# Performance work log

Hardware: AMD Instinct MI355X
Metric: run time of the kernel (lower is better)

The kernel has to match this reference:

```python
import jax, jax.numpy as jnp
import numpy as np

N = 100000
E = 1600000
F_IN = 128
H = 128


def setup_inputs() -> dict:
    key = jax.random.key(0)
    ks = jax.random.split(key, 12)
    x = jax.random.normal(ks[0], (N, F_IN), dtype=jnp.float32)
    edge_index = jax.random.randint(ks[1], (2, E), 0, N, dtype=jnp.int64)
    s = 1.0 / np.sqrt(F_IN)
    sh = 1.0 / np.sqrt(H)
    inp = {"x": x, "edge_index": edge_index}
    # SAGEConv params: lin_l (neighbor agg, with bias), lin_r (root, no bias)
    inp["W1l"] = jax.random.uniform(ks[2], (H, F_IN), jnp.float32, -s, s)
    inp["b1"] = jnp.zeros((H,), jnp.float32)
    inp["W1r"] = jax.random.uniform(ks[3], (H, F_IN), jnp.float32, -s, s)
    inp["W2l"] = jax.random.uniform(ks[4], (H, H), jnp.float32, -sh, sh)
    inp["b2"] = jnp.zeros((H,), jnp.float32)
    inp["W2r"] = jax.random.uniform(ks[5], (H, H), jnp.float32, -sh, sh)
    inp["W3l"] = jax.random.uniform(ks[6], (H, H), jnp.float32, -sh, sh)
    inp["b3"] = jnp.zeros((H,), jnp.float32)
    inp["W3r"] = jax.random.uniform(ks[7], (H, H), jnp.float32, -sh, sh)
    inp["Wo"] = jax.random.uniform(ks[8], (1, H), jnp.float32, -sh, sh)
    inp["bo"] = jnp.zeros((1,), jnp.float32)
    return inp


def _sage_max(h, src, dst, Wl, bl, Wr):
    # max-aggregate source features at destination nodes (empty -> 0, as PyG)
    m = jax.ops.segment_max(h[src], dst, num_segments=N)  # [N, d]
    m = jnp.where(jnp.isfinite(m), m, jnp.zeros_like(m))
    return m @ Wl.T + bl + h @ Wr.T


def reference(x, edge_index, W1l, b1, W1r, W2l, b2, W2r, W3l, b3, W3r, Wo, bo):
    src, dst = edge_index[0], edge_index[1]
    h1 = jax.nn.elu(_sage_max(x, src, dst, W1l, b1, W1r))
    h2 = jax.nn.elu(_sage_max(h1, src, dst, W2l, b2, W2r)) + h1
    h3 = jax.nn.elu(_sage_max(h2, src, dst, W3l, b3, W3r)) + h2
    return jax.nn.sigmoid(h3 @ Wo.T + bo)  # [N, 1]
```

## Files before the change

kernel.cpp:

```cpp
#include <hip/hip_runtime.h>
#include <hip/hip_fp16.h>
#include <math.h>

#define HDIM 128

#define BSHIFT 7
#define BW 128
#define BCAP 4096
#define NBKMAX 1024
#define CHUNK 4096

typedef __attribute__((ext_vector_type(8))) _Float16 f16x8;
typedef __attribute__((ext_vector_type(2))) _Float16 f16x2;
typedef __attribute__((ext_vector_type(16))) float f32x16;
typedef unsigned int uint32;
typedef unsigned short u16;

__device__ __forceinline__ uint32 hmax2u(uint32 a, uint32 b) {
    f16x2 ha = __builtin_bit_cast(f16x2, a);
    f16x2 hb = __builtin_bit_cast(f16x2, b);
    f16x2 r = __builtin_elementwise_max(ha, hb);
    return __builtin_bit_cast(uint32, r);
}
__device__ __forceinline__ uint32 hadd2u(uint32 a, uint32 b) {
    f16x2 ha = __builtin_bit_cast(f16x2, a);
    f16x2 hb = __builtin_bit_cast(f16x2, b);
    f16x2 r = ha + hb;
    return __builtin_bit_cast(uint32, r);
}


__global__ __launch_bounds__(256) void bucket_bin(
    const int* __restrict__ ei, int E_, int nbk,
    int* __restrict__ bucketCnt, uint32* __restrict__ tmp)
{
    __shared__ int cnt[NBKMAX];
    __shared__ int gbase[NBKMAX];
    const int t = threadIdx.x;
    const int start = blockIdx.x * CHUNK;
    const int end = min(start + CHUNK, E_);

    for (int i = t; i < nbk; i += 256) cnt[i] = 0;
    __syncthreads();
    for (int e = start + t; e < end; e += 256)
        atomicAdd(&cnt[ei[E_ + e] >> BSHIFT], 1);
    __syncthreads();
    for (int i = t; i < nbk; i += 256) {
        int c = cnt[i];
        gbase[i] = c ? atomicAdd(&bucketCnt[i], c) : 0;
    }
    __syncthreads();
    for (int i = t; i < nbk; i += 256) cnt[i] = 0;
    __syncthreads();
    for (int e = start + t; e < end; e += 256) {
        int d = ei[E_ + e];
        int s = ei[e];
        int b = d >> BSHIFT;
        int r = atomicAdd(&cnt[b], 1);
        tmp[(size_t)b * BCAP + gbase[b] + r] =
            ((uint32)(d & (BW - 1)) << 17) | (uint32)s;
    }
}

__global__ __launch_bounds__(1024) void bucket_scan(
    const int* __restrict__ bucketCnt, int* __restrict__ bucketBase,
    int nbk, int* __restrict__ off, int N_, int E_) {
    __shared__ int sd[1024];
    int t = threadIdx.x;
    int v = (t < nbk) ? bucketCnt[t] : 0;
    sd[t] = v;
    __syncthreads();
    for (int ofs = 1; ofs < 1024; ofs <<= 1) {
        int add = (t >= ofs) ? sd[t - ofs] : 0;
        __syncthreads();
        sd[t] += add;
        __syncthreads();
    }
    if (t < nbk) bucketBase[t] = sd[t] - v;
    if (t == 0) off[N_] = E_;
}

__global__ __launch_bounds__(256) void bucket_csr(
    const uint32* __restrict__ tmp, const int* __restrict__ bucketCnt,
    const int* __restrict__ bucketBase,
    int* __restrict__ off, int* __restrict__ srcs, int N_)
{
    __shared__ int lc[BW];
    __shared__ int lo[BW];
    __shared__ int sd[256];
    const int b = blockIdx.x, t = threadIdx.x;
    const int cnt = bucketCnt[b], base = bucketBase[b];
    const uint32* tp = tmp + (size_t)b * BCAP;

    if (t < BW) lc[t] = 0;
    __syncthreads();
    for (int i = t; i < cnt; i += 256) atomicAdd(&lc[tp[i] >> 17], 1);
    __syncthreads();

    int v = (t < BW) ? lc[t] : 0;
    sd[t] = v;
    __syncthreads();
    for (int ofs = 1; ofs < 256; ofs <<= 1) {
        int add = (t >= ofs) ? sd[t - ofs] : 0;
        __syncthreads();
        sd[t] += add;
        __syncthreads();
    }
    if (t < BW) lo[t] = sd[t] - v;
    __syncthreads();

    for (int i = t; i < BW; i += 256) {
        int node = b * BW + i;
        if (node < N_) off[node] = base + lo[i];
    }
    if (t < BW) lc[t] = lo[t];
    __syncthreads();
    for (int i = t; i < cnt; i += 256) {
        uint32 p = tp[i];
        int dl = p >> 17, s = p & 0x1FFFF;
        int pos = base + atomicAdd(&lc[dl], 1);
        srcs[pos] = s;
    }
}


__global__ void cast_x(const float* __restrict__ x, uint32* __restrict__ xb, int n2) {
    int i = blockIdx.x * 256 + threadIdx.x;
    if (i >= n2) return;
    float2 v = ((const float2*)x)[i];
    f16x2 h = { (_Float16)v.x, (_Float16)v.y };
    xb[i] = __builtin_bit_cast(uint32, h);
}

__global__ void cast_weights_packed(
    const float* __restrict__ W1l, const float* __restrict__ W1r,
    const float* __restrict__ W2l, const float* __restrict__ W2r,
    const float* __restrict__ W3l, const float* __restrict__ W3r,
    f16x8* __restrict__ PW)
{
    int tid = blockIdx.x * 256 + threadIdx.x;
    if (tid >= 3 * 4096) return;
    int layer = tid >> 12, rem = tid & 4095;
    int g = rem >> 10, ks = (rem >> 6) & 15, lane = rem & 63;
    int col = g * 32 + (lane & 31), kq = lane >> 5;
    const float* src;
    if (layer == 0)      src = (ks < 8) ? W1l : W1r;
    else if (layer == 1) src = (ks < 8) ? W2l : W2r;
    else                 src = (ks < 8) ? W3l : W3r;
    int kk = (ks & 7) * 16 + kq * 8;
    f16x8 v;
#pragma unroll
    for (int j = 0; j < 8; ++j) v[j] = (_Float16)src[col * HDIM + kk + j];
    PW[tid] = v;
}


#define ESTRIDE 136

__global__ __launch_bounds__(256, 8) void fused_layer(
    const uint32* __restrict__ hb,
    const int* __restrict__ off, const int* __restrict__ srcs,
    uint4* __restrict__ outb,
    const uint4* __restrict__ PW,
    const float* __restrict__ bias,
    int use_res,
    const float* __restrict__ Wo, const float* __restrict__ bo,
    float* __restrict__ out, int n_nodes)
{
    __shared__ alignas(16) char smemA[32 * ESTRIDE * 2];
    __shared__ uint4 sh[512];
    uint4*     sm = (uint4*)smemA;
    _Float16*  ho = (_Float16*)smemA;

    const int t = threadIdx.x, lane = t & 63, w = t >> 6;
    const int base = blockIdx.x * 32;
    const int l31 = lane & 31, kq = lane >> 5;
    const uint4* hp = (const uint4*)hb;

#pragma unroll
    for (int r = 0; r < 2; ++r) {
        int g = r * 256 + t;
        int row = g >> 4, c = g & 15;
        sh[row * 16 + (c ^ (row & 7))] = hp[(size_t)(base + row) * 16 + c];
    }

    const int es = lane >> 4, ch = lane & 15;
    const uint32 NINF = 0xFC00FC00u;
    for (int i = 0; i < 8; ++i) {
        const int row = w * 8 + i;
        const int node = base + row;
        int e0 = 0, e1 = 0;
        if (node < n_nodes) { e0 = off[node]; e1 = off[node + 1]; }
        uint32 m0 = NINF, m1 = NINF, m2 = NINF, m3 = NINF;

        int e = e0 + es;
        for (; e + 12 < e1; e += 16) {
            int s0 = srcs[e], s1 = srcs[e + 4], s2 = srcs[e + 8], s3 = srcs[e + 12];
            uint4 v0 = hp[(size_t)s0 * 16 + ch];
            uint4 v1 = hp[(size_t)s1 * 16 + ch];
            uint4 v2 = hp[(size_t)s2 * 16 + ch];
            uint4 v3 = hp[(size_t)s3 * 16 + ch];
            m0 = hmax2u(m0, v0.x); m1 = hmax2u(m1, v0.y);
            m2 = hmax2u(m2, v0.z); m3 = hmax2u(m3, v0.w);
            m0 = hmax2u(m0, v1.x); m1 = hmax2u(m1, v1.y);
            m2 = hmax2u(m2, v1.z); m3 = hmax2u(m3, v1.w);
            m0 = hmax2u(m0, v2.x); m1 = hmax2u(m1, v2.y);
            m2 = hmax2u(m2, v2.z); m3 = hmax2u(m3, v2.w);
            m0 = hmax2u(m0, v3.x); m1 = hmax2u(m1, v3.y);
            m2 = hmax2u(m2, v3.z); m3 = hmax2u(m3, v3.w);
        }
        for (; e < e1; e += 4) {
            uint4 v0 = hp[(size_t)srcs[e] * 16 + ch];
            m0 = hmax2u(m0, v0.x); m1 = hmax2u(m1, v0.y);
            m2 = hmax2u(m2, v0.z); m3 = hmax2u(m3, v0.w);
        }

        m0 = hmax2u(m0, __shfl_xor(m0, 16)); m0 = hmax2u(m0, __shfl_xor(m0, 32));
        m1 = hmax2u(m1, __shfl_xor(m1, 16)); m1 = hmax2u(m1, __shfl_xor(m1, 32));
        m2 = hmax2u(m2, __shfl_xor(m2, 16)); m2 = hmax2u(m2, __shfl_xor(m2, 32));
        m3 = hmax2u(m3, __shfl_xor(m3, 16)); m3 = hmax2u(m3, __shfl_xor(m3, 32));

        if (es == 0) {
            uint4 rr = make_uint4(0u, 0u, 0u, 0u);
            if (e1 > e0) { rr.x = m0; rr.y = m1; rr.z = m2; rr.w = m3; }
            sm[row * 16 + (ch ^ (row & 7))] = rr;
        }
    }
    __syncthreads();

    f32x16 acc = {};
#pragma unroll
    for (int k = 0; k < 8; ++k) {
        f16x8 a = __builtin_bit_cast(f16x8, sm[l31 * 16 + ((2 * k + kq) ^ (l31 & 7))]);
        f16x8 b = __builtin_bit_cast(f16x8, PW[(w * 16 + k) * 64 + lane]);
        acc = __builtin_amdgcn_mfma_f32_32x32x16_f16(a, b, acc, 0, 0, 0);
    }
#pragma unroll
    for (int k = 0; k < 8; ++k) {
        f16x8 a = __builtin_bit_cast(f16x8, sh[l31 * 16 + ((2 * k + kq) ^ (l31 & 7))]);
        f16x8 b = __builtin_bit_cast(f16x8, PW[(w * 16 + 8 + k) * 64 + lane]);
        acc = __builtin_amdgcn_mfma_f32_32x32x16_f16(a, b, acc, 0, 0, 0);
    }

    __syncthreads();

    const int C = w * 32 + l31;
    const float bv = bias[C];
#pragma unroll
    for (int r = 0; r < 16; ++r) {
        int row = (r & 3) + 8 * (r >> 2) + 4 * kq;
        float v = acc[r] + bv;
        v = (v > 0.f) ? v : (__expf(v) - 1.f);
        ho[row * ESTRIDE + C] = (_Float16)v;
    }
    __syncthreads();

#pragma unroll
    for (int r = 0; r < 2; ++r) {
        int g = r * 256 + t;
        int row = g >> 4, c = g & 15;
        int R = base + row;
        bool valid = (R < n_nodes);
        uint4 v = *(const uint4*)&ho[row * ESTRIDE + c * 8];
        if (use_res) {
            uint4 rv = sh[row * 16 + (c ^ (row & 7))];
            v.x = hadd2u(v.x, rv.x); v.y = hadd2u(v.y, rv.y);
            v.z = hadd2u(v.z, rv.z); v.w = hadd2u(v.w, rv.w);
        }
        if (outb) {
            if (valid) outb[(size_t)R * 16 + c] = v;
        } else {
            const float* wo = Wo + c * 8;
            f16x2 a0 = __builtin_bit_cast(f16x2, v.x);
            f16x2 a1 = __builtin_bit_cast(f16x2, v.y);
            f16x2 a2 = __builtin_bit_cast(f16x2, v.z);
            f16x2 a3 = __builtin_bit_cast(f16x2, v.w);
            float s = (float)a0.x * wo[0] + (float)a0.y * wo[1]
                    + (float)a1.x * wo[2] + (float)a1.y * wo[3]
                    + (float)a2.x * wo[4] + (float)a2.y * wo[5]
                    + (float)a3.x * wo[6] + (float)a3.y * wo[7];
#pragma unroll
            for (int o = 8; o; o >>= 1) s += __shfl_down(s, o, 16);
            if (valid && (t & 15) == 0)
                out[R] = 1.f / (1.f + expf(-(s + bo[0])));
        }
    }
}


extern "C" void kernel_launch(void* const* d_in, const int* in_sizes, int n_in,
                              void* d_out, int out_size, void* d_ws, size_t ws_size,
                              hipStream_t stream) {
    const float* x   = (const float*)d_in[0];
    const int*   ei  = (const int*)d_in[1];
    const float* W1l = (const float*)d_in[2];
    const float* b1  = (const float*)d_in[3];
    const float* W1r = (const float*)d_in[4];
    const float* W2l = (const float*)d_in[5];
    const float* b2  = (const float*)d_in[6];
    const float* W2r = (const float*)d_in[7];
    const float* W3l = (const float*)d_in[8];
    const float* b3  = (const float*)d_in[9];
    const float* W3r = (const float*)d_in[10];
    const float* Wo  = (const float*)d_in[11];
    const float* bo  = (const float*)d_in[12];
    float* out = (float*)d_out;

    const int N_ = in_sizes[0] / HDIM;
    const int E_ = in_sizes[1] / 2;
    const int Np = (N_ + 127) & ~127;
    const int nbk = (N_ + BW - 1) / BW;

    size_t o = 0;
    auto carve = [&](size_t bytes) { size_t r = o; o = (o + bytes + 255) & ~255ULL; return r; };
    char* ws = (char*)d_ws;
    int* off        = (int*)(ws + carve((size_t)(N_ + 1) * 4));
    int* bucketCnt  = (int*)(ws + carve((size_t)NBKMAX * 4));
    int* bucketBase = (int*)(ws + carve((size_t)NBKMAX * 4));
    int* srcs       = (int*)(ws + carve((size_t)E_ * 4));
    uint32* tmp     = (uint32*)(ws + carve((size_t)nbk * BCAP * 4));
    uint4* PW       = (uint4*)(ws + carve((size_t)3 * 4096 * 16));
    uint32* XB      = (uint32*)(ws + carve((size_t)Np * 64 * 4));
    uint32* H1B     = (uint32*)(ws + carve((size_t)Np * 64 * 4));
    (void)ws_size; (void)n_in; (void)out_size;

    (void)hipMemsetAsync(bucketCnt, 0, (size_t)NBKMAX * 4, stream);
    bucket_bin<<<(E_ + CHUNK - 1) / CHUNK, 256, 0, stream>>>(ei, E_, nbk, bucketCnt, tmp);
    bucket_scan<<<1, 1024, 0, stream>>>(bucketCnt, bucketBase, nbk, off, N_, E_);
    bucket_csr<<<nbk, 256, 0, stream>>>(tmp, bucketCnt, bucketBase, off, srcs, N_);

    cast_weights_packed<<<(3 * 4096 + 255) / 256, 256, 0, stream>>>(
        W1l, W1r, W2l, W2r, W3l, W3r, (f16x8*)PW);
    cast_x<<<(N_ * 64 + 255) / 256, 256, 0, stream>>>(x, XB, N_ * 64);

    const int nbF = (N_ + 31) / 32;

    const uint4* PW1 = PW;
    const uint4* PW2 = PW + 4096;
    const uint4* PW3 = PW + 8192;

    fused_layer<<<nbF, 256, 0, stream>>>(XB, off, srcs, (uint4*)H1B, PW1, b1,
                                         0, nullptr, nullptr, nullptr, N_);
    fused_layer<<<nbF, 256, 0, stream>>>(H1B, off, srcs, (uint4*)XB, PW2, b2,
                                         1, nullptr, nullptr, nullptr, N_);
    fused_layer<<<nbF, 256, 0, stream>>>(XB, off, srcs, nullptr, PW3, b3,
                                         1, Wo, bo, out, N_);
}
```

Before: 376.1 us.

## Stage block edge lists in LDS and software-pipeline neighbor gathers across rows

Before aggregation, the block's CSR offsets and source indices are copied into shared memory, with a fallback to global reads when the edge count exceeds a fixed cap. The per-row max gather becomes a double-buffered loop that issues the next row's first batch of feature loads while reducing the current row. Tail edges are clamped to the last valid index rather than handled by a separate remainder loop. The aim is to hide dependent index-then-feature load latency and cut redundant global index reads, at the cost of more registers, extra LDS and an added barrier.

```diff
diff --git a/kernel.cpp b/kernel.cpp
--- a/kernel.cpp
+++ b/kernel.cpp
@@ -156,6 +156,75 @@
 
 
 #define ESTRIDE 136
+#define EDGE_CAP 832
+
+#define RED16(m0,m1,m2,m3,V) do { \
+    m0 = hmax2u(m0, (V)[0].x); m1 = hmax2u(m1, (V)[0].y); \
+    m2 = hmax2u(m2, (V)[0].z); m3 = hmax2u(m3, (V)[0].w); \
+    m0 = hmax2u(m0, (V)[1].x); m1 = hmax2u(m1, (V)[1].y); \
+    m2 = hmax2u(m2, (V)[1].z); m3 = hmax2u(m3, (V)[1].w); \
+    m0 = hmax2u(m0, (V)[2].x); m1 = hmax2u(m1, (V)[2].y); \
+    m2 = hmax2u(m2, (V)[2].z); m3 = hmax2u(m3, (V)[2].w); \
+    m0 = hmax2u(m0, (V)[3].x); m1 = hmax2u(m1, (V)[3].y); \
+    m2 = hmax2u(m2, (V)[3].z); m3 = hmax2u(m3, (V)[3].w); \
+} while (0)
+
+template<bool L>
+__device__ __forceinline__ void issue_batch(
+    const uint4* __restrict__ hp, const int* __restrict__ srcs,
+    const int* sedge, int estart, int eb, int e1, int es, int ch, uint4* v)
+{
+    int last = e1 - 1;
+#pragma unroll
+    for (int k = 0; k < 4; ++k) {
+        int idx = min(eb + es + 4 * k, last);
+        int s = L ? sedge[idx - estart] : srcs[idx];
+        v[k] = hp[(size_t)s * 16 + ch];
+    }
+}
+
+template<bool L>
+__device__ __forceinline__ void gather8(
+    const uint4* __restrict__ hp, const int* __restrict__ srcs,
+    const int* sedge, int estart, int offv, int es, int ch, int w,
+    uint4* sm)
+{
+    const uint32 NINF = 0xFC00FC00u;
+    uint4 vb[2][4];
+
+    int e0 = __shfl(offv, 0), e1 = __shfl(offv, 1);
+    bool has = e1 > e0;
+    if (has) issue_batch<L>(hp, srcs, sedge, estart, e0, e1, es, ch, vb[0]);
+
+#pragma unroll
+    for (int i = 0; i < 8; ++i) {
+        int e0n = 0, e1n = 0; bool hasn = false;
+        if (i + 1 < 8) {
+            e0n = __shfl(offv, i + 1); e1n = __shfl(offv, i + 2);
+            hasn = e1n > e0n;
+            if (hasn) issue_batch<L>(hp, srcs, sedge, estart, e0n, e1n, es, ch, vb[(i + 1) & 1]);
+        }
+        uint32 m0 = NINF, m1 = NINF, m2 = NINF, m3 = NINF;
+        if (has) {
+            RED16(m0, m1, m2, m3, vb[i & 1]);
+            for (int eb = e0 + 16; eb < e1; eb += 16) {
+                issue_batch<L>(hp, srcs, sedge, estart, eb, e1, es, ch, vb[i & 1]);
+                RED16(m0, m1, m2, m3, vb[i & 1]);
+            }
+        }
+        m0 = hmax2u(m0, __shfl_xor(m0, 16)); m0 = hmax2u(m0, __shfl_xor(m0, 32));
+        m1 = hmax2u(m1, __shfl_xor(m1, 16)); m1 = hmax2u(m1, __shfl_xor(m1, 32));
+        m2 = hmax2u(m2, __shfl_xor(m2, 16)); m2 = hmax2u(m2, __shfl_xor(m2, 32));
+        m3 = hmax2u(m3, __shfl_xor(m3, 16)); m3 = hmax2u(m3, __shfl_xor(m3, 32));
+        if (es == 0) {
+            int row = w * 8 + i;
+            uint4 rr = make_uint4(0u, 0u, 0u, 0u);
+            if (has) { rr.x = m0; rr.y = m1; rr.z = m2; rr.w = m3; }
+            sm[row * 16 + (ch ^ (row & 7))] = rr;
+        }
+        e0 = e0n; e1 = e1n; has = hasn;
+    }
+}
 
 __global__ __launch_bounds__(256, 8) void fused_layer(
     const uint32* __restrict__ hb,
@@ -169,6 +238,8 @@
 {
     __shared__ alignas(16) char smemA[32 * ESTRIDE * 2];
     __shared__ uint4 sh[512];
+    __shared__ int soff[33];
+    __shared__ int sedge[EDGE_CAP];
     uint4*     sm = (uint4*)smemA;
     _Float16*  ho = (_Float16*)smemA;
 
@@ -177,6 +248,8 @@
     const int l31 = lane & 31, kq = lane >> 5;
     const uint4* hp = (const uint4*)hb;
 
+    if (t < 33) soff[t] = off[min(base + t, n_nodes)];
+
 #pragma unroll
     for (int r = 0; r < 2; ++r) {
         int g = r * 256 + t;
@@ -184,48 +257,18 @@
         sh[row * 16 + (c ^ (row & 7))] = hp[(size_t)(base + row) * 16 + c];
     }
 
+    const int estart = off[base];
+    const int eend = off[min(base + 32, n_nodes)];
+    const int ecnt = eend - estart;
+    const bool useLds = (ecnt <= EDGE_CAP);
+    const int scount = useLds ? ecnt : 0;
+    for (int i = t; i < scount; i += 256) sedge[i] = srcs[estart + i];
+    __syncthreads();
+
     const int es = lane >> 4, ch = lane & 15;
-    const uint32 NINF = 0xFC00FC00u;
-    for (int i = 0; i < 8; ++i) {
-        const int row = w * 8 + i;
-        const int node = base + row;
-        int e0 = 0, e1 = 0;
-        if (node < n_nodes) { e0 = off[node]; e1 = off[node + 1]; }
-        uint32 m0 = NINF, m1 = NINF, m2 = NINF, m3 = NINF;
-
-        int e = e0 + es;
-        for (; e + 12 < e1; e += 16) {
-            int s0 = srcs[e], s1 = srcs[e + 4], s2 = srcs[e + 8], s3 = srcs[e + 12];
-            uint4 v0 = hp[(size_t)s0 * 16 + ch];
-            uint4 v1 = hp[(size_t)s1 * 16 + ch];
-            uint4 v2 = hp[(size_t)s2 * 16 + ch];
-            uint4 v3 = hp[(size_t)s3 * 16 + ch];
-            m0 = hmax2u(m0, v0.x); m1 = hmax2u(m1, v0.y);
-            m2 = hmax2u(m2, v0.z); m3 = hmax2u(m3, v0.w);
-            m0 = hmax2u(m0, v1.x); m1 = hmax2u(m1, v1.y);
-            m2 = hmax2u(m2, v1.z); m3 = hmax2u(m3, v1.w);
-            m0 = hmax2u(m0, v2.x); m1 = hmax2u(m1, v2.y);
-            m2 = hmax2u(m2, v2.z); m3 = hmax2u(m3, v2.w);
-            m0 = hmax2u(m0, v3.x); m1 = hmax2u(m1, v3.y);
-            m2 = hmax2u(m2, v3.z); m3 = hmax2u(m3, v3.w);
-        }
-        for (; e < e1; e += 4) {
-            uint4 v0 = hp[(size_t)srcs[e] * 16 + ch];
-            m0 = hmax2u(m0, v0.x); m1 = hmax2u(m1, v0.y);
-            m2 = hmax2u(m2, v0.z); m3 = hmax2u(m3, v0.w);
-        }
-
-        m0 = hmax2u(m0, __shfl_xor(m0, 16)); m0 = hmax2u(m0, __shfl_xor(m0, 32));
-        m1 = hmax2u(m1, __shfl_xor(m1, 16)); m1 = hmax2u(m1, __shfl_xor(m1, 32));
-        m2 = hmax2u(m2, __shfl_xor(m2, 16)); m2 = hmax2u(m2, __shfl_xor(m2, 32));
-        m3 = hmax2u(m3, __shfl_xor(m3, 16)); m3 = hmax2u(m3, __shfl_xor(m3, 32));
-
-        if (es == 0) {
-            uint4 rr = make_uint4(0u, 0u, 0u, 0u);
-            if (e1 > e0) { rr.x = m0; rr.y = m1; rr.z = m2; rr.w = m3; }
-            sm[row * 16 + (ch ^ (row & 7))] = rr;
-        }
-    }
+    const int offv = soff[w * 8 + min(lane, 8)];
+    if (useLds) gather8<true >(hp, srcs, sedge, estart, offv, es, ch, w, sm);
+    else        gather8<false>(hp, srcs, sedge, estart, offv, es, ch, w, sm);
     __syncthreads();
 
     f32x16 acc = {};
```

Result: faster. 368.3 us (-2.1%).

## Split gather from GEMM and shard features into column slices for cache locality

Applied to the files above, without the earlier changes.

Feature buffers move to a column-sharded layout with 8 shards of 32 bytes per node. Max-aggregation now runs in a separate gather kernel, one block per (node tile, shard), with edge indices staged in LDS. Each shard's working set is about 3.2 MB, so the random gathers are meant to hit in L2 rather than pull full 256-byte rows. A separate GEMM kernel then reads the aggregated buffer. The trade is an extra global round trip for the aggregated features, three more launches, and reading the edge lists once per shard.

```diff
diff --git a/kernel.cpp b/kernel.cpp
--- a/kernel.cpp
+++ b/kernel.cpp
@@ -13,6 +13,7 @@
 typedef __attribute__((ext_vector_type(8))) _Float16 f16x8;
 typedef __attribute__((ext_vector_type(2))) _Float16 f16x2;
 typedef __attribute__((ext_vector_type(16))) float f32x16;
+typedef __attribute__((ext_vector_type(4))) unsigned int u32x4;
 typedef unsigned int uint32;
 typedef unsigned short u16;
 
@@ -27,6 +28,14 @@
     f16x2 hb = __builtin_bit_cast(f16x2, b);
     f16x2 r = ha + hb;
     return __builtin_bit_cast(uint32, r);
+}
+__device__ __forceinline__ uint32 pack2(float a, float b) {
+    f16x2 h = { (_Float16)a, (_Float16)b };
+    return __builtin_bit_cast(uint32, h);
+}
+__device__ __forceinline__ void nt_store4(uint4 v, uint4* p) {
+    u32x4 x = { v.x, v.y, v.z, v.w };
+    __builtin_nontemporal_store(x, (u32x4*)p);
 }
 
 
@@ -124,12 +133,17 @@
 }
 
 
-__global__ void cast_x(const float* __restrict__ x, uint32* __restrict__ xb, int n2) {
-    int i = blockIdx.x * 256 + threadIdx.x;
-    if (i >= n2) return;
-    float2 v = ((const float2*)x)[i];
-    f16x2 h = { (_Float16)v.x, (_Float16)v.y };
-    xb[i] = __builtin_bit_cast(uint32, h);
+__global__ void cast_x(const float* __restrict__ x, uint4* __restrict__ FB,
+                       int Np2, int n_nodes) {
+    int tid = blockIdx.x * 256 + threadIdx.x;
+    if (tid >= n_nodes * 16) return;
+    int node = tid >> 4, c = tid & 15;
+    const float4* xp = (const float4*)(x + (size_t)node * HDIM + c * 8);
+    float4 a = xp[0], b = xp[1];
+    uint4 v;
+    v.x = pack2(a.x, a.y); v.y = pack2(a.z, a.w);
+    v.z = pack2(b.x, b.y); v.w = pack2(b.z, b.w);
+    FB[(size_t)(c >> 1) * Np2 + node * 2 + (c & 1)] = v;
 }
 
 __global__ void cast_weights_packed(
@@ -155,17 +169,81 @@
 }
 
 
+#define GT 128
+#define GEC 3072
+
+template<bool L>
+__device__ __forceinline__ uint4 node_max(
+    const uint4* __restrict__ FS, const int* __restrict__ srcs,
+    const int* sedge, int estart, int e0, int deg, int half)
+{
+    const uint32 NINF = 0xFC00FC00u;
+    uint4 m = make_uint4(NINF, NINF, NINF, NINF);
+    int s = L ? sedge[e0 - estart] : srcs[e0];
+    uint4 v = FS[(size_t)s * 2 + half];
+    for (int k = 1; k < deg; ++k) {
+        int s2 = L ? sedge[e0 + k - estart] : srcs[e0 + k];
+        uint4 v2 = FS[(size_t)s2 * 2 + half];
+        m.x = hmax2u(m.x, v.x); m.y = hmax2u(m.y, v.y);
+        m.z = hmax2u(m.z, v.z); m.w = hmax2u(m.w, v.w);
+        v = v2;
+    }
+    m.x = hmax2u(m.x, v.x); m.y = hmax2u(m.y, v.y);
+    m.z = hmax2u(m.z, v.z); m.w = hmax2u(m.w, v.w);
+    return m;
+}
+
+__global__ __launch_bounds__(256, 8) void gather_shard(
+    const uint4* __restrict__ FB,
+    uint4* __restrict__ MB,
+    const int* __restrict__ off, const int* __restrict__ srcs,
+    int Np2, int n_nodes)
+{
+    __shared__ int soff[GT + 1];
+    __shared__ int sedge[GEC];
+    const int bid = blockIdx.x;
+    const int shard = bid & 7;
+    const int base = (bid >> 3) * GT;
+    const int t = threadIdx.x, lane = t & 63, w = t >> 6;
+
+    if (t <= GT) soff[t] = off[min(base + t, n_nodes)];
+    __syncthreads();
+    const int estart = soff[0], eend = soff[GT];
+    const int ecnt = eend - estart;
+    const bool useLds = (ecnt <= GEC);
+    if (useLds)
+        for (int i = t; i < ecnt; i += 256)
+            sedge[i] = __builtin_nontemporal_load(&srcs[estart + i]);
+    __syncthreads();
+
+    const uint4* FS = FB + (size_t)shard * Np2;
+    uint4*       MS = MB + (size_t)shard * Np2;
+
+    const int nl = w * 32 + (lane >> 1);
+    const int half = lane & 1;
+    const int node = base + nl;
+    const int e0 = soff[nl], deg = soff[nl + 1] - e0;
+
+    uint4 rr = make_uint4(0u, 0u, 0u, 0u);
+    if (deg > 0)
+        rr = useLds ? node_max<true >(FS, srcs, sedge, estart, e0, deg, half)
+                    : node_max<false>(FS, srcs, sedge, estart, e0, deg, half);
+    if (node < n_nodes)
+        nt_store4(rr, &MS[(size_t)node * 2 + half]);
+}
+
+
 #define ESTRIDE 136
 
-__global__ __launch_bounds__(256, 8) void fused_layer(
-    const uint32* __restrict__ hb,
-    const int* __restrict__ off, const int* __restrict__ srcs,
+__global__ __launch_bounds__(256, 8) void gemm_layer(
+    const uint4* __restrict__ mb,
+    const uint4* __restrict__ hb,
     uint4* __restrict__ outb,
     const uint4* __restrict__ PW,
     const float* __restrict__ bias,
     int use_res,
     const float* __restrict__ Wo, const float* __restrict__ bo,
-    float* __restrict__ out, int n_nodes)
+    float* __restrict__ out, int Np2, int n_nodes)
 {
     __shared__ alignas(16) char smemA[32 * ESTRIDE * 2];
     __shared__ uint4 sh[512];
@@ -175,56 +253,15 @@
     const int t = threadIdx.x, lane = t & 63, w = t >> 6;
     const int base = blockIdx.x * 32;
     const int l31 = lane & 31, kq = lane >> 5;
-    const uint4* hp = (const uint4*)hb;
 
 #pragma unroll
     for (int r = 0; r < 2; ++r) {
         int g = r * 256 + t;
         int row = g >> 4, c = g & 15;
-        sh[row * 16 + (c ^ (row & 7))] = hp[(size_t)(base + row) * 16 + c];
-    }
-
-    const int es = lane >> 4, ch = lane & 15;
-    const uint32 NINF = 0xFC00FC00u;
-    for (int i = 0; i < 8; ++i) {
-        const int row = w * 8 + i;
-        const int node = base + row;
-        int e0 = 0, e1 = 0;
-        if (node < n_nodes) { e0 = off[node]; e1 = off[node + 1]; }
-        uint32 m0 = NINF, m1 = NINF, m2 = NINF, m3 = NINF;
-
-        int e = e0 + es;
-        for (; e + 12 < e1; e += 16) {
-            int s0 = srcs[e], s1 = srcs[e + 4], s2 = srcs[e + 8], s3 = srcs[e + 12];
-            uint4 v0 = hp[(size_t)s0 * 16 + ch];
-            uint4 v1 = hp[(size_t)s1 * 16 + ch];
-            uint4 v2 = hp[(size_t)s2 * 16 + ch];
-            uint4 v3 = hp[(size_t)s3 * 16 + ch];
-            m0 = hmax2u(m0, v0.x); m1 = hmax2u(m1, v0.y);
-            m2 = hmax2u(m2, v0.z); m3 = hmax2u(m3, v0.w);
-            m0 = hmax2u(m0, v1.x); m1 = hmax2u(m1, v1.y);
-            m2 = hmax2u(m2, v1.z); m3 = hmax2u(m3, v1.w);
-            m0 = hmax2u(m0, v2.x); m1 = hmax2u(m1, v2.y);
-            m2 = hmax2u(m2, v2.z); m3 = hmax2u(m3, v2.w);
-            m0 = hmax2u(m0, v3.x); m1 = hmax2u(m1, v3.y);
-            m2 = hmax2u(m2, v3.z); m3 = hmax2u(m3, v3.w);
-        }
-        for (; e < e1; e += 4) {
-            uint4 v0 = hp[(size_t)srcs[e] * 16 + ch];
-            m0 = hmax2u(m0, v0.x); m1 = hmax2u(m1, v0.y);
-            m2 = hmax2u(m2, v0.z); m3 = hmax2u(m3, v0.w);
-        }
-
-        m0 = hmax2u(m0, __shfl_xor(m0, 16)); m0 = hmax2u(m0, __shfl_xor(m0, 32));
-        m1 = hmax2u(m1, __shfl_xor(m1, 16)); m1 = hmax2u(m1, __shfl_xor(m1, 32));
-        m2 = hmax2u(m2, __shfl_xor(m2, 16)); m2 = hmax2u(m2, __shfl_xor(m2, 32));
-        m3 = hmax2u(m3, __shfl_xor(m3, 16)); m3 = hmax2u(m3, __shfl_xor(m3, 32));
-
-        if (es == 0) {
-            uint4 rr = make_uint4(0u, 0u, 0u, 0u);
-            if (e1 > e0) { rr.x = m0; rr.y = m1; rr.z = m2; rr.w = m3; }
-            sm[row * 16 + (ch ^ (row & 7))] = rr;
-        }
+        size_t gi = (size_t)(c >> 1) * Np2 + (size_t)(base + row) * 2 + (c & 1);
+        int sw = c ^ (row & 7);
+        sm[row * 16 + sw] = mb[gi];
+        sh[row * 16 + sw] = hb[gi];
     }
     __syncthreads();
 
@@ -268,7 +305,8 @@
             v.z = hadd2u(v.z, rv.z); v.w = hadd2u(v.w, rv.w);
         }
         if (outb) {
-            if (valid) outb[(size_t)R * 16 + c] = v;
+            if (valid)
+                outb[(size_t)(c >> 1) * Np2 + (size_t)R * 2 + (c & 1)] = v;
         } else {
             const float* wo = Wo + c * 8;
             f16x2 a0 = __builtin_bit_cast(f16x2, v.x);
@@ -309,6 +347,7 @@
     const int N_ = in_sizes[0] / HDIM;
     const int E_ = in_sizes[1] / 2;
     const int Np = (N_ + 127) & ~127;
+    const int Np2 = Np * 2;
     const int nbk = (N_ + BW - 1) / BW;
 
     size_t o = 0;
@@ -320,8 +359,9 @@
     int* srcs       = (int*)(ws + carve((size_t)E_ * 4));
     uint32* tmp     = (uint32*)(ws + carve((size_t)nbk * BCAP * 4));
     uint4* PW       = (uint4*)(ws + carve((size_t)3 * 4096 * 16));
-    uint32* XB      = (uint32*)(ws + carve((size_t)Np * 64 * 4));
-    uint32* H1B     = (uint32*)(ws + carve((size_t)Np * 64 * 4));
+    uint4* XB       = (uint4*)(ws + carve((size_t)Np * 256));
+    uint4* H1B      = (uint4*)(ws + carve((size_t)Np * 256));
+    uint4* MB       = (uint4*)(ws + carve((size_t)Np * 256));
     (void)ws_size; (void)n_in; (void)out_size;
 
     (void)hipMemsetAsync(bucketCnt, 0, (size_t)NBKMAX * 4, stream);
@@ -331,18 +371,23 @@
 
     cast_weights_packed<<<(3 * 4096 + 255) / 256, 256, 0, stream>>>(
         W1l, W1r, W2l, W2r, W3l, W3r, (f16x8*)PW);
-    cast_x<<<(N_ * 64 + 255) / 256, 256, 0, stream>>>(x, XB, N_ * 64);
-
-    const int nbF = (N_ + 31) / 32;
+    cast_x<<<(N_ * 16 + 255) / 256, 256, 0, stream>>>(x, XB, Np2, N_);
+
+    const int ntile = (N_ + GT - 1) / GT;
+    const int nbG = ntile * 8;
+    const int nbM = Np / 32;
 
     const uint4* PW1 = PW;
     const uint4* PW2 = PW + 4096;
     const uint4* PW3 = PW + 8192;
 
-    fused_layer<<<nbF, 256, 0, stream>>>(XB, off, srcs, (uint4*)H1B, PW1, b1,
-                                         0, nullptr, nullptr, nullptr, N_);
-    fused_layer<<<nbF, 256, 0, stream>>>(H1B, off, srcs, (uint4*)XB, PW2, b2,
-                                         1, nullptr, nullptr, nullptr, N_);
-    fused_layer<<<nbF, 256, 0, stream>>>(XB, off, srcs, nullptr, PW3, b3,
-                                         1, Wo, bo, out, N_);
-}
+    gather_shard<<<nbG, 256, 0, stream>>>(XB, MB, off, srcs, Np2, N_);
+    gemm_layer<<<nbM, 256, 0, stream>>>(MB, XB, H1B, PW1, b1,
+                                        0, nullptr, nullptr, nullptr, Np2, N_);
+    gather_shard<<<nbG, 256, 0, stream>>>(H1B, MB, off, srcs, Np2, N_);
+    gemm_layer<<<nbM, 256, 0, stream>>>(MB, H1B, XB, PW2, b2,
+                                        1, nullptr, nullptr, nullptr, Np2, N_);
+    gather_shard<<<nbG, 256, 0, stream>>>(XB, MB, off, srcs, Np2, N_);
+    gemm_layer<<<nbM, 256, 0, stream>>>(MB, XB, nullptr, PW3, b3,
+                                        1, Wo, bo, out, Np2, N_);
+}
```

Measured after the change: 464.5 us. 23.5% more time.
